# Kernel optimization log

Hardware: AMD Instinct MI355X
Metric: run time of the kernel (lower is better)

Reference implementation:

```python
import jax, jax.numpy as jnp
import numpy as np

N_NODES = 100000
N_EDGES = 600000
IN_DIM = 128
HID = 128
OUT_DIM = 64
N_LAYERS = 3


def setup_inputs() -> dict:
    key = jax.random.key(0)
    ks = jax.random.split(key, 8)
    x = jax.random.normal(ks[0], (N_NODES, IN_DIM), dtype=jnp.float32)
    edge_index = jax.random.randint(ks[1], (2, N_EDGES), 0, N_NODES, dtype=jnp.int64)
    s = 1.0 / np.sqrt(HID)
    W_in = jax.random.normal(ks[2], (HID, IN_DIM), dtype=jnp.float32) * s
    b_in = jax.random.normal(ks[3], (HID,), dtype=jnp.float32) * s
    W_convs = jax.random.normal(ks[4], (N_LAYERS, HID, HID), dtype=jnp.float32) * s
    b_convs = jax.random.normal(ks[5], (N_LAYERS, HID), dtype=jnp.float32) * s
    W_out = jax.random.normal(ks[6], (OUT_DIM, (N_LAYERS + 1) * HID), dtype=jnp.float32) * s
    b_out = jax.random.normal(ks[7], (OUT_DIM,), dtype=jnp.float32) * s
    return {"x": x, "edge_index": edge_index, "W_in": W_in, "b_in": b_in,
            "W_convs": W_convs, "b_convs": b_convs, "W_out": W_out, "b_out": b_out}


def reference(x, edge_index, W_in, b_in, W_convs, b_convs, W_out, b_out):
    src, dst = edge_index[0], edge_index[1]
    n = x.shape[0]
    # input projection: [N, in] -> [N, H]
    h = x @ W_in.T + b_in
    hidden_states = [h]
    for i in range(W_convs.shape[0]):
        # GINConv (eps=0): nn(x + sum of neighbor messages), messages src->dst
        agg = jax.ops.segment_sum(h[src], dst, num_segments=n)
        h = (h + agg) @ W_convs[i].T + b_convs[i]
        hidden_states.append(h)
    cat = jnp.concatenate(hidden_states, axis=1)  # [N, (L+1)*H]
    out = cat @ W_out.T + b_out  # [N, OUT]
    return jax.nn.softmax(out, axis=-1)
```

## Files before the change

### kernel.cpp

```cpp
#include <hip/hip_runtime.h>
#include <hip/hip_bf16.h>
#include <hip/hip_fp16.h>

#define GN 100000
#define GE 600000
#define SCAN_NBLK 98
#define ALD 132

typedef __bf16    bf16x8 __attribute__((ext_vector_type(8)));
typedef __bf16    bf16x4 __attribute__((ext_vector_type(4)));
typedef _Float16  f16x8  __attribute__((ext_vector_type(8)));
typedef float     f32x4  __attribute__((ext_vector_type(4)));

__global__ __launch_bounds__(256) void convert_w(
    const float* __restrict__ Win, const float* __restrict__ Wc,
    const float* __restrict__ Wout,
    __bf16* __restrict__ hi, __bf16* __restrict__ lo)
{
    const int i = blockIdx.x * 256 + threadIdx.x;
    if (i >= 98304) return;
    float v;
    if (i < 16384)      v = Win[i];
    else if (i < 65536) v = Wc[i - 16384];
    else                v = Wout[i - 65536];
    const __bf16 h = (__bf16)v;
    hi[i] = h;
    lo[i] = (__bf16)(v - (float)h);
}

__device__ __forceinline__ void gather8_f16(
    const uint* __restrict__ Hw,
    const int* __restrict__ row_start,
    const int* __restrict__ deg,
    const int* __restrict__ csr,
    const int row0, const int wave, const int lane,
    float* __restrict__ Acc)
{
    float2 acc8[8];
    int start8[8], deg8[8];
    int maxd = 0;
#pragma unroll
    for (int r = 0; r < 8; ++r) {
        acc8[r] = make_float2(0.f, 0.f);
        const int v = row0 + wave * 8 + r;
        start8[r] = (v < GN) ? row_start[v] : 0;
        deg8[r]   = (v < GN) ? deg[v] : 0;
        maxd = max(maxd, deg8[r]);
    }

    for (int b = 0; b < maxd; b += 64) {
        int idx8[8];
#pragma unroll
        for (int r = 0; r < 8; ++r) {
            const int off = max(min(b + lane, deg8[r] - 1), 0);
            idx8[r] = min(max(csr[start8[r] + off], 0), GN - 1);
        }
        const int wend = min(maxd - b, 64);
        for (int c = 0; c < wend; c += 4) {
            uint t[8][4];
#pragma unroll
            for (int cc = 0; cc < 4; ++cc) {
#pragma unroll
                for (int r = 0; r < 8; ++r) {
                    const int s = __shfl(idx8[r], c + cc);
                    t[r][cc] = Hw[(size_t)s * 64 + lane];
                }
            }
#pragma unroll
            for (int cc = 0; cc < 4; ++cc) {
                const int k = b + c + cc;
#pragma unroll
                for (int r = 0; r < 8; ++r) {
                    const float m = (k < deg8[r]) ? 1.f : 0.f;
                    union { uint u; _Float16 h[2]; } cv;
                    cv.u = t[r][cc];
                    acc8[r].x = fmaf(m, (float)cv.h[0], acc8[r].x);
                    acc8[r].y = fmaf(m, (float)cv.h[1], acc8[r].y);
                }
            }
        }
    }

    __syncthreads();
    const int j = lane * 2;
#pragma unroll
    for (int r = 0; r < 8; ++r) {
        float* a = &Acc[(wave * 8 + r) * ALD + j];
        a[0] += acc8[r].x;
        a[1] += acc8[r].y;
    }
}

template<bool GATHER>
__global__ __launch_bounds__(256, 4) void gin_layer(
    const float* __restrict__ H, int ldH,
    const _Float16* __restrict__ HfIn,
    const int* __restrict__ row_start,
    const int* __restrict__ deg,
    const int* __restrict__ csr,
    const __bf16* __restrict__ Whi,
    const __bf16* __restrict__ Wlo,
    const float* __restrict__ bias,
    float* __restrict__ C, int ldC,
    _Float16* __restrict__ HfOut)
{
    constexpr int K = 128;

    __shared__ float Acc[32 * ALD];

    const int tid  = threadIdx.x;
    const int wave = tid >> 6;
    const int lane = tid & 63;
    const int row0 = blockIdx.x * 32;
    const int wn   = wave * 32;
    const int quad = lane >> 4;
    const int l15  = lane & 15;

#pragma unroll
    for (int p = 0; p < 4; ++p) {
        const int q  = tid + p * 256;
        const int r  = q >> 5;
        const int c4 = (q & 31) * 4;
        float4 v = make_float4(0.f, 0.f, 0.f, 0.f);
        if (row0 + r < GN) v = *(const float4*)(H + (size_t)(row0 + r) * ldH + c4);
        *(float4*)&Acc[r * ALD + c4] = v;
    }

    if (GATHER)
        gather8_f16((const uint*)HfIn, row_start, deg, csr, row0, wave, lane, Acc);
    __syncthreads();

    f32x4 acc[2][2];
#pragma unroll
    for (int i = 0; i < 2; ++i)
#pragma unroll
        for (int j = 0; j < 2; ++j) acc[i][j] = (f32x4)(0.0f);

#pragma unroll
    for (int ks = 0; ks < 4; ++ks) {
        const int kt = ks * 32 + quad * 8;
        bf16x8 ahi[2], alo[2];
#pragma unroll
        for (int mt = 0; mt < 2; ++mt) {
            const float* ap = &Acc[(mt * 16 + l15) * ALD + kt];
            const f32x4 p = *(const f32x4*)ap;
            const f32x4 q = *(const f32x4*)(ap + 4);
#pragma unroll
            for (int e = 0; e < 4; ++e) {
                const __bf16 hp = (__bf16)p[e];
                const __bf16 hq = (__bf16)q[e];
                ahi[mt][e]     = hp;
                ahi[mt][e + 4] = hq;
                alo[mt][e]     = (__bf16)(p[e] - (float)hp);
                alo[mt][e + 4] = (__bf16)(q[e] - (float)hq);
            }
        }
        bf16x8 whi[2], wlo[2];
#pragma unroll
        for (int nt = 0; nt < 2; ++nt) {
            const int n = wn + nt * 16 + l15;
            whi[nt] = *(const bf16x8*)(Whi + (size_t)n * K + kt);
            wlo[nt] = *(const bf16x8*)(Wlo + (size_t)n * K + kt);
        }
#pragma unroll
        for (int mt = 0; mt < 2; ++mt)
#pragma unroll
            for (int nt = 0; nt < 2; ++nt) {
                acc[mt][nt] = __builtin_amdgcn_mfma_f32_16x16x32_bf16(
                    ahi[mt], whi[nt], acc[mt][nt], 0, 0, 0);
                acc[mt][nt] = __builtin_amdgcn_mfma_f32_16x16x32_bf16(
                    ahi[mt], wlo[nt], acc[mt][nt], 0, 0, 0);
                acc[mt][nt] = __builtin_amdgcn_mfma_f32_16x16x32_bf16(
                    alo[mt], whi[nt], acc[mt][nt], 0, 0, 0);
            }
    }
    __syncthreads();

#pragma unroll
    for (int nt = 0; nt < 2; ++nt) {
        const int col = wn + nt * 16 + l15;
        const float b = bias[col];
#pragma unroll
        for (int mt = 0; mt < 2; ++mt)
#pragma unroll
            for (int r4 = 0; r4 < 4; ++r4)
                Acc[(mt * 16 + quad * 4 + r4) * ALD + col] = acc[mt][nt][r4] + b;
    }
    __syncthreads();
#pragma unroll
    for (int p = 0; p < 4; ++p) {
        const int q  = tid + p * 256;
        const int r  = q >> 5;
        const int c4 = (q & 31) * 4;
        const int gr = row0 + r;
        if (gr < GN)
            *(float4*)(C + (size_t)gr * ldC + c4) = *(const float4*)&Acc[r * ALD + c4];
    }
#pragma unroll
    for (int p = 0; p < 2; ++p) {
        const int q = tid + p * 256;
        const int r = q >> 4;
        const int g = (q & 15) * 8;
        const int gr = row0 + r;
        if (gr < GN) {
            const float4 a = *(const float4*)&Acc[r * ALD + g];
            const float4 b = *(const float4*)&Acc[r * ALD + g + 4];
            f16x8 o = {(_Float16)a.x, (_Float16)a.y, (_Float16)a.z, (_Float16)a.w,
                       (_Float16)b.x, (_Float16)b.y, (_Float16)b.z, (_Float16)b.w};
            *(f16x8*)&HfOut[(size_t)gr * 128 + g] = o;
        }
    }
}

__global__ __launch_bounds__(256, 4) void gin_final(
    const float* __restrict__ cat3,
    const _Float16* __restrict__ HfIn,
    const int* __restrict__ row_start,
    const int* __restrict__ deg,
    const int* __restrict__ csr,
    const __bf16* __restrict__ Whi3,
    const __bf16* __restrict__ Wlo3,
    const float* __restrict__ b3,
    const __bf16* __restrict__ WhiO,
    const __bf16* __restrict__ WloO,
    const float* __restrict__ bO,
    float* __restrict__ out)
{
    constexpr int CLD = 68;

    __shared__ float Smem[32 * ALD];
    float* const Acc = Smem;
    float* const Cst = Smem;

    const int tid  = threadIdx.x;
    const int wave = tid >> 6;
    const int lane = tid & 63;
    const int row0 = blockIdx.x * 32;
    const int quad = lane >> 4;
    const int l15  = lane & 15;

#pragma unroll
    for (int p = 0; p < 4; ++p) {
        const int q  = tid + p * 256;
        const int r  = q >> 5;
        const int c4 = (q & 31) * 4;
        float4 v = make_float4(0.f, 0.f, 0.f, 0.f);
        if (row0 + r < GN)
            v = *(const float4*)(cat3 + (size_t)(row0 + r) * 384 + 256 + c4);
        *(float4*)&Acc[r * ALD + c4] = v;
    }

    gather8_f16((const uint*)HfIn, row_start, deg, csr, row0, wave, lane, Acc);
    __syncthreads();

    const int wn = wave * 32;
    f32x4 acc1[2][2];
#pragma unroll
    for (int i = 0; i < 2; ++i)
#pragma unroll
        for (int j = 0; j < 2; ++j) acc1[i][j] = (f32x4)(0.0f);

#pragma unroll
    for (int ks = 0; ks < 4; ++ks) {
        const int kt = ks * 32 + quad * 8;
        bf16x8 ahi[2], alo[2];
#pragma unroll
        for (int mt = 0; mt < 2; ++mt) {
            const float* ap = &Acc[(mt * 16 + l15) * ALD + kt];
            const f32x4 p = *(const f32x4*)ap;
            const f32x4 q = *(const f32x4*)(ap + 4);
#pragma unroll
            for (int e = 0; e < 4; ++e) {
                const __bf16 hp = (__bf16)p[e];
                const __bf16 hq = (__bf16)q[e];
                ahi[mt][e]     = hp;
                ahi[mt][e + 4] = hq;
                alo[mt][e]     = (__bf16)(p[e] - (float)hp);
                alo[mt][e + 4] = (__bf16)(q[e] - (float)hq);
            }
        }
        bf16x8 whi[2], wlo[2];
#pragma unroll
        for (int nt = 0; nt < 2; ++nt) {
            const int n = wn + nt * 16 + l15;
            whi[nt] = *(const bf16x8*)(Whi3 + (size_t)n * 128 + kt);
            wlo[nt] = *(const bf16x8*)(Wlo3 + (size_t)n * 128 + kt);
        }
#pragma unroll
        for (int mt = 0; mt < 2; ++mt)
#pragma unroll
            for (int nt = 0; nt < 2; ++nt) {
                acc1[mt][nt] = __builtin_amdgcn_mfma_f32_16x16x32_bf16(
                    ahi[mt], whi[nt], acc1[mt][nt], 0, 0, 0);
                acc1[mt][nt] = __builtin_amdgcn_mfma_f32_16x16x32_bf16(
                    ahi[mt], wlo[nt], acc1[mt][nt], 0, 0, 0);
                acc1[mt][nt] = __builtin_amdgcn_mfma_f32_16x16x32_bf16(
                    alo[mt], whi[nt], acc1[mt][nt], 0, 0, 0);
            }
    }
    __syncthreads();

#pragma unroll
    for (int nt = 0; nt < 2; ++nt) {
        const int col = wn + nt * 16 + l15;
        const float b = b3[col];
#pragma unroll
        for (int mt = 0; mt < 2; ++mt)
#pragma unroll
            for (int r4 = 0; r4 < 4; ++r4)
                Acc[(mt * 16 + quad * 4 + r4) * ALD + col] = acc1[mt][nt][r4] + b;
    }
    __syncthreads();

    const int wk  = wave & 1;
    const int wn2 = (wave >> 1) * 32;
    f32x4 acc2[2][2];
#pragma unroll
    for (int i = 0; i < 2; ++i)
#pragma unroll
        for (int j = 0; j < 2; ++j) acc2[i][j] = (f32x4)(0.0f);

#pragma unroll
    for (int ks = 0; ks < 8; ++ks) {
        const int kg = wk * 256 + ks * 32 + quad * 8;
        bf16x8 ahi[2], alo[2];
#pragma unroll
        for (int mt = 0; mt < 2; ++mt) {
            const int row = mt * 16 + l15;
            f32x4 p, q;
            if (kg < 384) {
                const float* ap = cat3 + (size_t)(row0 + row) * 384 + kg;
                p = *(const f32x4*)ap;
                q = *(const f32x4*)(ap + 4);
            } else {
                const float* ap = &Acc[row * ALD + (kg - 384)];
                p = *(const f32x4*)ap;
                q = *(const f32x4*)(ap + 4);
            }
#pragma unroll
            for (int e = 0; e < 4; ++e) {
                const __bf16 hp = (__bf16)p[e];
                const __bf16 hq = (__bf16)q[e];
                ahi[mt][e]     = hp;
                ahi[mt][e + 4] = hq;
                alo[mt][e]     = (__bf16)(p[e] - (float)hp);
                alo[mt][e + 4] = (__bf16)(q[e] - (float)hq);
            }
        }
        bf16x8 whi[2], wlo[2];
#pragma unroll
        for (int nt = 0; nt < 2; ++nt) {
            const int n = wn2 + nt * 16 + l15;
            whi[nt] = *(const bf16x8*)(WhiO + (size_t)n * 512 + kg);
            wlo[nt] = *(const bf16x8*)(WloO + (size_t)n * 512 + kg);
        }
#pragma unroll
        for (int mt = 0; mt < 2; ++mt)
#pragma unroll
            for (int nt = 0; nt < 2; ++nt) {
                acc2[mt][nt] = __builtin_amdgcn_mfma_f32_16x16x32_bf16(
                    ahi[mt], whi[nt], acc2[mt][nt], 0, 0, 0);
                acc2[mt][nt] = __builtin_amdgcn_mfma_f32_16x16x32_bf16(
                    ahi[mt], wlo[nt], acc2[mt][nt], 0, 0, 0);
                acc2[mt][nt] = __builtin_amdgcn_mfma_f32_16x16x32_bf16(
                    alo[mt], whi[nt], acc2[mt][nt], 0, 0, 0);
            }
    }

    __syncthreads();

    if (wk == 1) {
#pragma unroll
        for (int nt = 0; nt < 2; ++nt)
#pragma unroll
            for (int mt = 0; mt < 2; ++mt)
#pragma unroll
                for (int r4 = 0; r4 < 4; ++r4)
                    Cst[(mt * 16 + quad * 4 + r4) * CLD + wn2 + nt * 16 + l15]
                        = acc2[mt][nt][r4];
    }
    __syncthreads();
    if (wk == 0) {
#pragma unroll
        for (int nt = 0; nt < 2; ++nt) {
            const int col = wn2 + nt * 16 + l15;
            const float b = bO[col];
#pragma unroll
            for (int mt = 0; mt < 2; ++mt)
#pragma unroll
                for (int r4 = 0; r4 < 4; ++r4) {
                    const int idx = (mt * 16 + quad * 4 + r4) * CLD + col;
                    Cst[idx] = Cst[idx] + acc2[mt][nt][r4] + b;
                }
        }
    }
    __syncthreads();

    for (int i = 0; i < 8; ++i) {
        const int r = wave * 8 + i;
        const float v = Cst[r * CLD + lane];
        float m = v;
#pragma unroll
        for (int off = 32; off > 0; off >>= 1) m = fmaxf(m, __shfl_xor(m, off));
        const float e = __expf(v - m);
        float s = e;
#pragma unroll
        for (int off = 32; off > 0; off >>= 1) s += __shfl_xor(s, off);
        const int gr = row0 + r;
        if (gr < GN) out[(size_t)gr * 64 + lane] = e / s;
    }
}

__global__ __launch_bounds__(256) void count_deg(const int* __restrict__ dst,
                                                 int* __restrict__ deg)
{
    const int e = blockIdx.x * 256 + threadIdx.x;
    if (e < GE) atomicAdd(&deg[dst[e]], 1);
}

__global__ __launch_bounds__(256) void scan_pass1(const int* __restrict__ deg,
                                                  int* __restrict__ excl,
                                                  int* __restrict__ blockSums)
{
    __shared__ int s[256];
    const int t = threadIdx.x;
    const int base = blockIdx.x * 1024 + t * 4;

    int4 v = make_int4(0, 0, 0, 0);
    if (base + 3 < GN) {
        v = *(const int4*)(deg + base);
    } else {
        if (base + 0 < GN) v.x = deg[base + 0];
        if (base + 1 < GN) v.y = deg[base + 1];
        if (base + 2 < GN) v.z = deg[base + 2];
        if (base + 3 < GN) v.w = deg[base + 3];
    }
    const int mysum = v.x + v.y + v.z + v.w;
    s[t] = mysum;
    __syncthreads();
    for (int off = 1; off < 256; off <<= 1) {
        const int val = (t >= off) ? s[t - off] : 0;
        __syncthreads();
        s[t] += val;
        __syncthreads();
    }
    int4 o;
    o.x = s[t] - mysum;
    o.y = o.x + v.x;
    o.z = o.y + v.y;
    o.w = o.z + v.z;
    if (base + 3 < GN) {
        *(int4*)(excl + base) = o;
    } else {
        if (base + 0 < GN) excl[base + 0] = o.x;
        if (base + 1 < GN) excl[base + 1] = o.y;
        if (base + 2 < GN) excl[base + 2] = o.z;
        if (base + 3 < GN) excl[base + 3] = o.w;
    }
    if (t == 255) blockSums[blockIdx.x] = s[255];
}

__global__ __launch_bounds__(128) void scan_pass2(const int* __restrict__ blockSums,
                                                  int* __restrict__ blockOffs, int n)
{
    __shared__ int s[128];
    const int t = threadIdx.x;
    const int v = (t < n) ? blockSums[t] : 0;
    s[t] = v;
    __syncthreads();
    for (int off = 1; off < 128; off <<= 1) {
        const int val = (t >= off) ? s[t - off] : 0;
        __syncthreads();
        s[t] += val;
        __syncthreads();
    }
    if (t < n) blockOffs[t] = s[t] - v;
}

__global__ __launch_bounds__(256) void scan_pass3(int* __restrict__ excl,
                                                  const int* __restrict__ blockOffs,
                                                  int* __restrict__ cursor)
{
    const int i = blockIdx.x * 256 + threadIdx.x;
    if (i >= GN) return;
    const int v = excl[i] + blockOffs[i >> 10];
    excl[i]   = v;
    cursor[i] = v;
}

__global__ __launch_bounds__(256) void fill_csr(const int* __restrict__ src,
                                                const int* __restrict__ dst,
                                                int* __restrict__ cursor,
                                                int* __restrict__ csr)
{
    const int e = blockIdx.x * 256 + threadIdx.x;
    if (e >= GE) return;
    const int pos = atomicAdd(&cursor[dst[e]], 1);
    csr[pos] = src[e];
}

extern "C" void kernel_launch(void* const* d_in, const int* in_sizes, int n_in,
                              void* d_out, int out_size, void* d_ws, size_t ws_size,
                              hipStream_t stream)
{
    const float* x       = (const float*)d_in[0];
    const int*   src     = (const int*)d_in[1];
    const int*   dst     = ((const int*)d_in[1]) + GE;
    const float* W_in    = (const float*)d_in[2];
    const float* b_in    = (const float*)d_in[3];
    const float* W_convs = (const float*)d_in[4];
    const float* b_convs = (const float*)d_in[5];
    const float* W_out   = (const float*)d_in[6];
    const float* b_out   = (const float*)d_in[7];
    float*       out     = (float*)d_out;

    float*    cat3 = (float*)d_ws;
    _Float16* Hf0  = (_Float16*)(cat3 + (size_t)GN * 384);
    _Float16* Hf1  = Hf0 + (size_t)GN * 128;
    int*      deg       = (int*)(Hf1 + (size_t)GN * 128);
    int*      row_start = deg + GN;
    int*      cursor    = row_start + GN;
    int*      blockSums = cursor + GN;
    int*      blockOffs = blockSums + 128;
    int*      csr       = blockOffs + 128;
    __bf16*   Whi       = (__bf16*)(csr + GE);
    __bf16*   Wlo       = Whi + 98304;

    const dim3 blk(256);
    const dim3 gblk(256);
    const int edge_blocks  = (GE + 255) / 256;
    const int node_blocks  = (GN + 255) / 256;
    const int layer_blocks = (GN + 31) / 32;

    hipMemsetAsync(deg, 0, GN * sizeof(int), stream);
    count_deg<<<edge_blocks, blk, 0, stream>>>(dst, deg);
    scan_pass1<<<SCAN_NBLK, blk, 0, stream>>>(deg, row_start, blockSums);
    scan_pass2<<<1, 128, 0, stream>>>(blockSums, blockOffs, SCAN_NBLK);
    scan_pass3<<<node_blocks, blk, 0, stream>>>(row_start, blockOffs, cursor);
    fill_csr<<<edge_blocks, blk, 0, stream>>>(src, dst, cursor, csr);

    convert_w<<<(98304 + 255) / 256, blk, 0, stream>>>(W_in, W_convs, W_out, Whi, Wlo);

    gin_layer<false><<<layer_blocks, gblk, 0, stream>>>(
        x, 128, nullptr, nullptr, nullptr, nullptr,
        Whi, Wlo, b_in, cat3, 384, Hf0);

    gin_layer<true><<<layer_blocks, gblk, 0, stream>>>(
        cat3, 384, Hf0, row_start, deg, csr,
        Whi + 16384, Wlo + 16384, b_convs, cat3 + 128, 384, Hf1);
    gin_layer<true><<<layer_blocks, gblk, 0, stream>>>(
        cat3 + 128, 384, Hf1, row_start, deg, csr,
        Whi + 32768, Wlo + 32768, b_convs + 128, cat3 + 256, 384, Hf0);

    gin_final<<<layer_blocks, gblk, 0, stream>>>(
        cat3, Hf0, row_start, deg, csr,
        Whi + 49152, Wlo + 49152, b_convs + 256,
        Whi + 65536, Wlo + 65536, b_out, out);
}
```

Before: 464.9 us.

## Software-pipeline weight/activation loads and widen gather batching in GIN kernels

Prefetches the next k-step's weight (and, in the output projection, activation) fragments into registers while the current MFMAs run. The neighbor gather now issues eight loads per row batch instead of four, and masks values with a select instead of a multiply-FMA. A __syncthreads is dropped, and occupancy is lowered to 3 blocks/SM to make room for the extra registers. Bounds checks are removed because GN is divisible by 32, which relies on the fixed problem size.

```diff
diff --git a/kernel.cpp b/kernel.cpp
--- a/kernel.cpp
+++ b/kernel.cpp
@@ -43,8 +43,8 @@
     for (int r = 0; r < 8; ++r) {
         acc8[r] = make_float2(0.f, 0.f);
         const int v = row0 + wave * 8 + r;
-        start8[r] = (v < GN) ? row_start[v] : 0;
-        deg8[r]   = (v < GN) ? deg[v] : 0;
+        start8[r] = row_start[v];
+        deg8[r]   = deg[v];
         maxd = max(maxd, deg8[r]);
     }
 
@@ -56,32 +56,27 @@
             idx8[r] = min(max(csr[start8[r] + off], 0), GN - 1);
         }
         const int wend = min(maxd - b, 64);
-        for (int c = 0; c < wend; c += 4) {
-            uint t[8][4];
-#pragma unroll
-            for (int cc = 0; cc < 4; ++cc) {
+        for (int c = 0; c < wend; c += 8) {
+            uint t[8][8];
+#pragma unroll
+            for (int cc = 0; cc < 8; ++cc)
+#pragma unroll
+                for (int r = 0; r < 8; ++r)
+                    t[cc][r] = Hw[(size_t)__shfl(idx8[r], c + cc) * 64 + lane];
+#pragma unroll
+            for (int cc = 0; cc < 8; ++cc) {
+                const int k = b + c + cc;
 #pragma unroll
                 for (int r = 0; r < 8; ++r) {
-                    const int s = __shfl(idx8[r], c + cc);
-                    t[r][cc] = Hw[(size_t)s * 64 + lane];
+                    union { uint u; _Float16 h[2]; } cv;
+                    cv.u = (k < deg8[r]) ? t[cc][r] : 0u;
+                    acc8[r].x += (float)cv.h[0];
+                    acc8[r].y += (float)cv.h[1];
                 }
             }
-#pragma unroll
-            for (int cc = 0; cc < 4; ++cc) {
-                const int k = b + c + cc;
-#pragma unroll
-                for (int r = 0; r < 8; ++r) {
-                    const float m = (k < deg8[r]) ? 1.f : 0.f;
-                    union { uint u; _Float16 h[2]; } cv;
-                    cv.u = t[r][cc];
-                    acc8[r].x = fmaf(m, (float)cv.h[0], acc8[r].x);
-                    acc8[r].y = fmaf(m, (float)cv.h[1], acc8[r].y);
-                }
-            }
-        }
-    }
-
-    __syncthreads();
+        }
+    }
+
     const int j = lane * 2;
 #pragma unroll
     for (int r = 0; r < 8; ++r) {
@@ -92,7 +87,7 @@
 }
 
 template<bool GATHER>
-__global__ __launch_bounds__(256, 4) void gin_layer(
+__global__ __launch_bounds__(256, 3) void gin_layer(
     const float* __restrict__ H, int ldH,
     const _Float16* __restrict__ HfIn,
     const int* __restrict__ row_start,
@@ -104,8 +99,6 @@
     float* __restrict__ C, int ldC,
     _Float16* __restrict__ HfOut)
 {
-    constexpr int K = 128;
-
     __shared__ float Acc[32 * ALD];
 
     const int tid  = threadIdx.x;
@@ -116,16 +109,21 @@
     const int quad = lane >> 4;
     const int l15  = lane & 15;
 
-#pragma unroll
-    for (int p = 0; p < 4; ++p) {
-        const int q  = tid + p * 256;
-        const int r  = q >> 5;
-        const int c4 = (q & 31) * 4;
-        float4 v = make_float4(0.f, 0.f, 0.f, 0.f);
-        if (row0 + r < GN) v = *(const float4*)(H + (size_t)(row0 + r) * ldH + c4);
-        *(float4*)&Acc[r * ALD + c4] = v;
-    }
-
+    {
+        const int sr = wave * 8 + (lane >> 5) ;
+        float4 sv[4];
+#pragma unroll
+        for (int p = 0; p < 4; ++p) {
+            const int r = wave * 8 + p * 2 + (lane >> 5);
+            sv[p] = *(const float4*)(H + (size_t)(row0 + r) * ldH + (lane & 31) * 4);
+        }
+#pragma unroll
+        for (int p = 0; p < 4; ++p) {
+            const int r = wave * 8 + p * 2 + (lane >> 5);
+            *(float4*)&Acc[r * ALD + (lane & 31) * 4] = sv[p];
+        }
+        (void)sr;
+    }
     if (GATHER)
         gather8_f16((const uint*)HfIn, row_start, deg, csr, row0, wave, lane, Acc);
     __syncthreads();
@@ -136,9 +134,26 @@
 #pragma unroll
         for (int j = 0; j < 2; ++j) acc[i][j] = (f32x4)(0.0f);
 
+    bf16x8 whA[2], wlA[2], whB[2], wlB[2];
+#pragma unroll
+    for (int nt = 0; nt < 2; ++nt) {
+        const int n = wn + nt * 16 + l15;
+        whA[nt] = *(const bf16x8*)(Whi + (size_t)n * 128 + quad * 8);
+        wlA[nt] = *(const bf16x8*)(Wlo + (size_t)n * 128 + quad * 8);
+    }
+
 #pragma unroll
     for (int ks = 0; ks < 4; ++ks) {
         const int kt = ks * 32 + quad * 8;
+        if (ks < 3) {
+            const int kn = kt + 32;
+#pragma unroll
+            for (int nt = 0; nt < 2; ++nt) {
+                const int n = wn + nt * 16 + l15;
+                whB[nt] = *(const bf16x8*)(Whi + (size_t)n * 128 + kn);
+                wlB[nt] = *(const bf16x8*)(Wlo + (size_t)n * 128 + kn);
+            }
+        }
         bf16x8 ahi[2], alo[2];
 #pragma unroll
         for (int mt = 0; mt < 2; ++mt) {
@@ -155,24 +170,24 @@
                 alo[mt][e + 4] = (__bf16)(q[e] - (float)hq);
             }
         }
-        bf16x8 whi[2], wlo[2];
-#pragma unroll
-        for (int nt = 0; nt < 2; ++nt) {
-            const int n = wn + nt * 16 + l15;
-            whi[nt] = *(const bf16x8*)(Whi + (size_t)n * K + kt);
-            wlo[nt] = *(const bf16x8*)(Wlo + (size_t)n * K + kt);
-        }
 #pragma unroll
         for (int mt = 0; mt < 2; ++mt)
 #pragma unroll
             for (int nt = 0; nt < 2; ++nt) {
                 acc[mt][nt] = __builtin_amdgcn_mfma_f32_16x16x32_bf16(
-                    ahi[mt], whi[nt], acc[mt][nt], 0, 0, 0);
+                    ahi[mt], whA[nt], acc[mt][nt], 0, 0, 0);
                 acc[mt][nt] = __builtin_amdgcn_mfma_f32_16x16x32_bf16(
-                    ahi[mt], wlo[nt], acc[mt][nt], 0, 0, 0);
+                    ahi[mt], wlA[nt], acc[mt][nt], 0, 0, 0);
                 acc[mt][nt] = __builtin_amdgcn_mfma_f32_16x16x32_bf16(
-                    alo[mt], whi[nt], acc[mt][nt], 0, 0, 0);
-            }
+                    alo[mt], whA[nt], acc[mt][nt], 0, 0, 0);
+            }
+        if (ks < 3) {
+#pragma unroll
+            for (int nt = 0; nt < 2; ++nt) {
+                whA[nt] = whB[nt];
+                wlA[nt] = wlB[nt];
+            }
+        }
     }
     __syncthreads();
 
@@ -192,27 +207,22 @@
         const int q  = tid + p * 256;
         const int r  = q >> 5;
         const int c4 = (q & 31) * 4;
-        const int gr = row0 + r;
-        if (gr < GN)
-            *(float4*)(C + (size_t)gr * ldC + c4) = *(const float4*)&Acc[r * ALD + c4];
+        *(float4*)(C + (size_t)(row0 + r) * ldC + c4) = *(const float4*)&Acc[r * ALD + c4];
     }
 #pragma unroll
     for (int p = 0; p < 2; ++p) {
         const int q = tid + p * 256;
         const int r = q >> 4;
         const int g = (q & 15) * 8;
-        const int gr = row0 + r;
-        if (gr < GN) {
-            const float4 a = *(const float4*)&Acc[r * ALD + g];
-            const float4 b = *(const float4*)&Acc[r * ALD + g + 4];
-            f16x8 o = {(_Float16)a.x, (_Float16)a.y, (_Float16)a.z, (_Float16)a.w,
-                       (_Float16)b.x, (_Float16)b.y, (_Float16)b.z, (_Float16)b.w};
-            *(f16x8*)&HfOut[(size_t)gr * 128 + g] = o;
-        }
-    }
-}
-
-__global__ __launch_bounds__(256, 4) void gin_final(
+        const float4 a = *(const float4*)&Acc[r * ALD + g];
+        const float4 b = *(const float4*)&Acc[r * ALD + g + 4];
+        f16x8 o = {(_Float16)a.x, (_Float16)a.y, (_Float16)a.z, (_Float16)a.w,
+                   (_Float16)b.x, (_Float16)b.y, (_Float16)b.z, (_Float16)b.w};
+        *(f16x8*)&HfOut[(size_t)(row0 + r) * 128 + g] = o;
+    }
+}
+
+__global__ __launch_bounds__(256, 3) void gin_final(
     const float* __restrict__ cat3,
     const _Float16* __restrict__ HfIn,
     const int* __restrict__ row_start,
@@ -239,17 +249,19 @@
     const int quad = lane >> 4;
     const int l15  = lane & 15;
 
-#pragma unroll
-    for (int p = 0; p < 4; ++p) {
-        const int q  = tid + p * 256;
-        const int r  = q >> 5;
-        const int c4 = (q & 31) * 4;
-        float4 v = make_float4(0.f, 0.f, 0.f, 0.f);
-        if (row0 + r < GN)
-            v = *(const float4*)(cat3 + (size_t)(row0 + r) * 384 + 256 + c4);
-        *(float4*)&Acc[r * ALD + c4] = v;
-    }
-
+    {
+        float4 sv[4];
+#pragma unroll
+        for (int p = 0; p < 4; ++p) {
+            const int r = wave * 8 + p * 2 + (lane >> 5);
+            sv[p] = *(const float4*)(cat3 + (size_t)(row0 + r) * 384 + 256 + (lane & 31) * 4);
+        }
+#pragma unroll
+        for (int p = 0; p < 4; ++p) {
+            const int r = wave * 8 + p * 2 + (lane >> 5);
+            *(float4*)&Acc[r * ALD + (lane & 31) * 4] = sv[p];
+        }
+    }
     gather8_f16((const uint*)HfIn, row_start, deg, csr, row0, wave, lane, Acc);
     __syncthreads();
 
@@ -260,43 +272,61 @@
 #pragma unroll
         for (int j = 0; j < 2; ++j) acc1[i][j] = (f32x4)(0.0f);
 
-#pragma unroll
-    for (int ks = 0; ks < 4; ++ks) {
-        const int kt = ks * 32 + quad * 8;
-        bf16x8 ahi[2], alo[2];
-#pragma unroll
-        for (int mt = 0; mt < 2; ++mt) {
-            const float* ap = &Acc[(mt * 16 + l15) * ALD + kt];
-            const f32x4 p = *(const f32x4*)ap;
-            const f32x4 q = *(const f32x4*)(ap + 4);
-#pragma unroll
-            for (int e = 0; e < 4; ++e) {
-                const __bf16 hp = (__bf16)p[e];
-                const __bf16 hq = (__bf16)q[e];
-                ahi[mt][e]     = hp;
-                ahi[mt][e + 4] = hq;
-                alo[mt][e]     = (__bf16)(p[e] - (float)hp);
-                alo[mt][e + 4] = (__bf16)(q[e] - (float)hq);
-            }
-        }
-        bf16x8 whi[2], wlo[2];
+    {
+        bf16x8 whA[2], wlA[2], whB[2], wlB[2];
 #pragma unroll
         for (int nt = 0; nt < 2; ++nt) {
             const int n = wn + nt * 16 + l15;
-            whi[nt] = *(const bf16x8*)(Whi3 + (size_t)n * 128 + kt);
-            wlo[nt] = *(const bf16x8*)(Wlo3 + (size_t)n * 128 + kt);
-        }
-#pragma unroll
-        for (int mt = 0; mt < 2; ++mt)
-#pragma unroll
-            for (int nt = 0; nt < 2; ++nt) {
-                acc1[mt][nt] = __builtin_amdgcn_mfma_f32_16x16x32_bf16(
-                    ahi[mt], whi[nt], acc1[mt][nt], 0, 0, 0);
-                acc1[mt][nt] = __builtin_amdgcn_mfma_f32_16x16x32_bf16(
-                    ahi[mt], wlo[nt], acc1[mt][nt], 0, 0, 0);
-                acc1[mt][nt] = __builtin_amdgcn_mfma_f32_16x16x32_bf16(
-                    alo[mt], whi[nt], acc1[mt][nt], 0, 0, 0);
-            }
+            whA[nt] = *(const bf16x8*)(Whi3 + (size_t)n * 128 + quad * 8);
+            wlA[nt] = *(const bf16x8*)(Wlo3 + (size_t)n * 128 + quad * 8);
+        }
+#pragma unroll
+        for (int ks = 0; ks < 4; ++ks) {
+            const int kt = ks * 32 + quad * 8;
+            if (ks < 3) {
+                const int kn = kt + 32;
+#pragma unroll
+                for (int nt = 0; nt < 2; ++nt) {
+                    const int n = wn + nt * 16 + l15;
+                    whB[nt] = *(const bf16x8*)(Whi3 + (size_t)n * 128 + kn);
+                    wlB[nt] = *(const bf16x8*)(Wlo3 + (size_t)n * 128 + kn);
+                }
+            }
+            bf16x8 ahi[2], alo[2];
+#pragma unroll
+            for (int mt = 0; mt < 2; ++mt) {
+                const float* ap = &Acc[(mt * 16 + l15) * ALD + kt];
+                const f32x4 p = *(const f32x4*)ap;
+                const f32x4 q = *(const f32x4*)(ap + 4);
+#pragma unroll
+                for (int e = 0; e < 4; ++e) {
+                    const __bf16 hp = (__bf16)p[e];
+                    const __bf16 hq = (__bf16)q[e];
+                    ahi[mt][e]     = hp;
+                    ahi[mt][e + 4] = hq;
+                    alo[mt][e]     = (__bf16)(p[e] - (float)hp);
+                    alo[mt][e + 4] = (__bf16)(q[e] - (float)hq);
+                }
+            }
+#pragma unroll
+            for (int mt = 0; mt < 2; ++mt)
+#pragma unroll
+                for (int nt = 0; nt < 2; ++nt) {
+                    acc1[mt][nt] = __builtin_amdgcn_mfma_f32_16x16x32_bf16(
+                        ahi[mt], whA[nt], acc1[mt][nt], 0, 0, 0);
+                    acc1[mt][nt] = __builtin_amdgcn_mfma_f32_16x16x32_bf16(
+                        ahi[mt], wlA[nt], acc1[mt][nt], 0, 0, 0);
+                    acc1[mt][nt] = __builtin_amdgcn_mfma_f32_16x16x32_bf16(
+                        alo[mt], whA[nt], acc1[mt][nt], 0, 0, 0);
+                }
+            if (ks < 3) {
+#pragma unroll
+                for (int nt = 0; nt < 2; ++nt) {
+                    whA[nt] = whB[nt];
+                    wlA[nt] = wlB[nt];
+                }
+            }
+        }
     }
     __syncthreads();
 
@@ -320,51 +350,80 @@
 #pragma unroll
         for (int j = 0; j < 2; ++j) acc2[i][j] = (f32x4)(0.0f);
 
-#pragma unroll
-    for (int ks = 0; ks < 8; ++ks) {
-        const int kg = wk * 256 + ks * 32 + quad * 8;
-        bf16x8 ahi[2], alo[2];
+    f32x4 pA[2], qA[2], pB[2], qB[2];
+    bf16x8 whA[2], wlA[2], whB[2], wlB[2];
+
+    {
+        const int kg = wk * 256 + quad * 8;
 #pragma unroll
         for (int mt = 0; mt < 2; ++mt) {
             const int row = mt * 16 + l15;
-            f32x4 p, q;
-            if (kg < 384) {
-                const float* ap = cat3 + (size_t)(row0 + row) * 384 + kg;
-                p = *(const f32x4*)ap;
-                q = *(const f32x4*)(ap + 4);
-            } else {
-                const float* ap = &Acc[row * ALD + (kg - 384)];
-                p = *(const f32x4*)ap;
-                q = *(const f32x4*)(ap + 4);
-            }
+            const float* ap = cat3 + (size_t)(row0 + row) * 384 + kg;
+            pA[mt] = *(const f32x4*)ap;
+            qA[mt] = *(const f32x4*)(ap + 4);
+        }
+#pragma unroll
+        for (int nt = 0; nt < 2; ++nt) {
+            const int n = wn2 + nt * 16 + l15;
+            whA[nt] = *(const bf16x8*)(WhiO + (size_t)n * 512 + kg);
+            wlA[nt] = *(const bf16x8*)(WloO + (size_t)n * 512 + kg);
+        }
+    }
+
+#pragma unroll
+    for (int ks = 0; ks < 8; ++ks) {
+        if (ks < 7) {
+            const int kg = wk * 256 + (ks + 1) * 32 + quad * 8;
+#pragma unroll
+            for (int mt = 0; mt < 2; ++mt) {
+                const int row = mt * 16 + l15;
+                if (kg < 384) {
+                    const float* ap = cat3 + (size_t)(row0 + row) * 384 + kg;
+                    pB[mt] = *(const f32x4*)ap;
+                    qB[mt] = *(const f32x4*)(ap + 4);
+                } else {
+                    const float* ap = &Acc[row * ALD + (kg - 384)];
+                    pB[mt] = *(const f32x4*)ap;
+                    qB[mt] = *(const f32x4*)(ap + 4);
+                }
+            }
+#pragma unroll
+            for (int nt = 0; nt < 2; ++nt) {
+                const int n = wn2 + nt * 16 + l15;
+                whB[nt] = *(const bf16x8*)(WhiO + (size_t)n * 512 + kg);
+                wlB[nt] = *(const bf16x8*)(WloO + (size_t)n * 512 + kg);
+            }
+        }
+        bf16x8 ahi[2], alo[2];
+#pragma unroll
+        for (int mt = 0; mt < 2; ++mt) {
 #pragma unroll
             for (int e = 0; e < 4; ++e) {
-                const __bf16 hp = (__bf16)p[e];
-                const __bf16 hq = (__bf16)q[e];
+                const __bf16 hp = (__bf16)pA[mt][e];
+                const __bf16 hq = (__bf16)qA[mt][e];
                 ahi[mt][e]     = hp;
                 ahi[mt][e + 4] = hq;
-                alo[mt][e]     = (__bf16)(p[e] - (float)hp);
-                alo[mt][e + 4] = (__bf16)(q[e] - (float)hq);
-            }
-        }
-        bf16x8 whi[2], wlo[2];
-#pragma unroll
-        for (int nt = 0; nt < 2; ++nt) {
-            const int n = wn2 + nt * 16 + l15;
-            whi[nt] = *(const bf16x8*)(WhiO + (size_t)n * 512 + kg);
-            wlo[nt] = *(const bf16x8*)(WloO + (size_t)n * 512 + kg);
+                alo[mt][e]     = (__bf16)(pA[mt][e] - (float)hp);
+                alo[mt][e + 4] = (__bf16)(qA[mt][e] - (float)hq);
+            }
         }
 #pragma unroll
         for (int mt = 0; mt < 2; ++mt)
 #pragma unroll
             for (int nt = 0; nt < 2; ++nt) {
                 acc2[mt][nt] = __builtin_amdgcn_mfma_f32_16x16x32_bf16(
-                    ahi[mt], whi[nt], acc2[mt][nt], 0, 0, 0);
+                    ahi[mt], whA[nt], acc2[mt][nt], 0, 0, 0);
                 acc2[mt][nt] = __builtin_amdgcn_mfma_f32_16x16x32_bf16(
-                    ahi[mt], wlo[nt], acc2[mt][nt], 0, 0, 0);
+                    ahi[mt], wlA[nt], acc2[mt][nt], 0, 0, 0);
                 acc2[mt][nt] = __builtin_amdgcn_mfma_f32_16x16x32_bf16(
-                    alo[mt], whi[nt], acc2[mt][nt], 0, 0, 0);
-            }
+                    alo[mt], whA[nt], acc2[mt][nt], 0, 0, 0);
+            }
+        if (ks < 7) {
+#pragma unroll
+            for (int mt = 0; mt < 2; ++mt) { pA[mt] = pB[mt]; qA[mt] = qB[mt]; }
+#pragma unroll
+            for (int nt = 0; nt < 2; ++nt) { whA[nt] = whB[nt]; wlA[nt] = wlB[nt]; }
+        }
     }
 
     __syncthreads();
@@ -406,8 +465,7 @@
         float s = e;
 #pragma unroll
         for (int off = 32; off > 0; off >>= 1) s += __shfl_xor(s, off);
-        const int gr = row0 + r;
-        if (gr < GN) out[(size_t)gr * 64 + lane] = e / s;
+        out[(size_t)(row0 + r) * 64 + lane] = e / s;
     }
 }
 
@@ -530,7 +588,7 @@
     const dim3 gblk(256);
     const int edge_blocks  = (GE + 255) / 256;
     const int node_blocks  = (GN + 255) / 256;
-    const int layer_blocks = (GN + 31) / 32;
+    const int layer_blocks = GN / 32;
 
     hipMemsetAsync(deg, 0, GN * sizeof(int), stream);
     count_deg<<<edge_blocks, blk, 0, stream>>>(dst, deg);
```

After: 473.1 us. About the same (+1.8%).
